# Kernel optimization log

Hardware: AMD Instinct MI355X
Metric: run time of the kernel (lower is better)

The kernel has to match this reference:

```python
import jax, jax.numpy as jnp
import numpy as np

N_ATOMS = 10000
N_EDGES = 200000
L_MAX = 2
K_L = [32, 24, 16]  # k_max_l = n_element_channels * n_max_l

# (l1, l2, L) in the original loop order (l1 outer, l2 inner, L ascending)
PAIRS = [(0,0,0),(0,1,1),(0,2,2),
         (1,0,1),(1,1,0),(1,1,1),(1,1,2),(1,2,1),(1,2,2),
         (2,0,2),(2,1,1),(2,1,2),(2,2,0),(2,2,1),(2,2,2)]
# concatenated input width -> k_max_l[L] per (L, sigma) channel
LIN = {'0_1': (72, 32), '1_1': (80, 24), '1_m1': (40, 24), '2_1': (72, 16), '2_m1': (32, 16)}


def setup_inputs() -> dict:
    key = jax.random.key(0)
    it = iter(jax.random.split(key, 64))
    def nrm(shape):
        return jax.random.normal(next(it), shape, dtype=jnp.float32)
    inp = {}
    for l in range(L_MAX + 1):
        inp['rb%d' % l] = nrm((N_EDGES, K_L[l]))           # radial basis per l
    for l in range(L_MAX + 1):
        inp['sh%d' % l] = nrm((N_EDGES, 2*l+1, 1))         # spherical harmonics per l
    inp['emb'] = nrm((N_ATOMS, 1, K_L[0]))                 # initial center embedding
    for l in range(L_MAX + 1):
        inp['f%d' % l] = nrm((N_ATOMS, 2*l+1, K_L[l]))     # nu=1 equivariant features
    for (l1, l2, L) in PAIRS:
        inp['cg_%d_%d_%d' % (l1, l2, L)] = nrm(((2*l1+1)*(2*l2+1), 2*L+1))
    for LS, (fin, fout) in LIN.items():
        inp['W_' + LS] = nrm((fin, fout)) / np.float32(np.sqrt(fin))
        inp['b_' + LS] = nrm((fout,)) * 0.01
    inp['centers'] = jax.random.randint(next(it), (N_EDGES,), 0, N_ATOMS)
    inp['neighbors'] = jax.random.randint(next(it), (N_EDGES,), 0, N_ATOMS)
    inp['n_atoms'] = N_ATOMS
    return inp


def _normalize(x, dims):
    # Normalizer(dims): RMS normalization over the given dims
    return x * jax.lax.rsqrt(jnp.mean(x * x, axis=dims, keepdims=True) + 1e-12)


def _forward(floats, centers, neighbors, n_atoms):
    (rb0, rb1, rb2, sh0, sh1, sh2, emb, f0, f1, f2,
     cg_0_0_0, cg_0_1_1, cg_0_2_2, cg_1_0_1, cg_1_1_0, cg_1_1_1, cg_1_1_2,
     cg_1_2_1, cg_1_2_2, cg_2_0_2, cg_2_1_1, cg_2_1_2, cg_2_2_0, cg_2_2_1,
     cg_2_2_2, W_0_1, b_0_1, W_1_1, b_1_1, W_1_m1, b_1_m1, W_2_1, b_2_1,
     W_2_m1, b_2_m1) = floats
    rb = [rb0, rb1, rb2]; sh = [sh0, sh1, sh2]; feats = [f0, f1, f2]
    cgs = {'0_0_0': cg_0_0_0, '0_1_1': cg_0_1_1, '0_2_2': cg_0_2_2,
           '1_0_1': cg_1_0_1, '1_1_0': cg_1_1_0, '1_1_1': cg_1_1_1,
           '1_1_2': cg_1_1_2, '1_2_1': cg_1_2_1, '1_2_2': cg_1_2_2,
           '2_0_2': cg_2_0_2, '2_1_1': cg_2_1_1, '2_1_2': cg_2_1_2,
           '2_2_0': cg_2_2_0, '2_2_1': cg_2_2_1, '2_2_2': cg_2_2_2}
    lin = {'0_1': (W_0_1, b_0_1), '1_1': (W_1_1, b_1_1), '1_m1': (W_1_m1, b_1_m1),
           '2_1': (W_2_1, b_2_1), '2_m1': (W_2_m1, b_2_m1)}

    # ---- InvariantMessagePasser: density_l = scatter_add over centers of
    #      sh_l * rb_l * emb[neighbors]
    emb_n = emb[neighbors]                                       # [E, 1, k0]
    densities = []
    for l in range(L_MAX + 1):
        msg = sh[l] * rb[l][:, None, :] * emb_n[:, :, :K_L[l]]   # [E, 2l+1, k_l]
        densities.append(jax.ops.segment_sum(msg, centers, num_segments=n_atoms))

    # ---- EquivariantMessagePasser
    ve = [sh[l] * rb[l][:, None, :] for l in range(L_MAX + 1)]   # vector expansion [E,2l+1,k_l]
    fn = [feats[l][neighbors] for l in range(L_MAX + 1)]         # gathered neighbor feats
    results = {}
    for (l1, l2, L) in PAIRS:
        S = (-1) ** (l1 + l2 + L)
        k = min(K_L[l1], K_L[l2])
        t1 = ve[l1][:, :, :k]                                    # [E, 2l1+1, k]
        t2 = fn[l2][:, :, :k]                                    # [E, 2l2+1, k]
        cg = cgs['%d_%d_%d' % (l1, l2, L)].reshape(2*l1+1, 2*l2+1, 2*L+1)
        # fused outer product + CG contraction -> [E, 2L+1, k]
        res = jnp.einsum('eak,ebk,abM->eMk', t1, t2, cg)
        pooled = jax.ops.segment_sum(res, centers, num_segments=n_atoms)
        LS = '%d_%s' % (L, 'm1' if S < 0 else '1')
        results.setdefault(LS, []).append(pooled)

    outs = {}
    for LS, (W, b) in lin.items():
        x = jnp.concatenate(results[LS], axis=2)                 # [n_atoms, 2L+1, size_LS]
        x = _normalize(x, (0, 1))
        x = jnp.einsum('amf,fk->amk', x, W) + b
        outs[LS] = _normalize(x, (0, 1, 2))

    return (densities[0], densities[1], densities[2],
            outs['0_1'], outs['1_1'], outs['1_m1'], outs['2_1'], outs['2_m1'])


def reference(rb0, rb1, rb2, sh0, sh1, sh2, emb, f0, f1, f2,
              cg_0_0_0, cg_0_1_1, cg_0_2_2, cg_1_0_1, cg_1_1_0, cg_1_1_1,
              cg_1_1_2, cg_1_2_1, cg_1_2_2, cg_2_0_2, cg_2_1_1, cg_2_1_2,
              cg_2_2_0, cg_2_2_1, cg_2_2_2, W_0_1, b_0_1, W_1_1, b_1_1,
              W_1_m1, b_1_m1, W_2_1, b_2_1, W_2_m1, b_2_m1,
              centers, neighbors, n_atoms):
    floats = (rb0, rb1, rb2, sh0, sh1, sh2, emb, f0, f1, f2,
              cg_0_0_0, cg_0_1_1, cg_0_2_2, cg_1_0_1, cg_1_1_0, cg_1_1_1,
              cg_1_1_2, cg_1_2_1, cg_1_2_2, cg_2_0_2, cg_2_1_1, cg_2_1_2,
              cg_2_2_0, cg_2_2_1, cg_2_2_2, W_0_1, b_0_1, W_1_1, b_1_1,
              W_1_m1, b_1_m1, W_2_1, b_2_1, W_2_m1, b_2_m1)
    return _forward(floats, centers, neighbors, n_atoms)
```

## Files before the change

kernel.cpp:

```cpp
#include <hip/hip_runtime.h>
#include <hip/hip_bf16.h>

typedef __hip_bfloat16 bf16;

#define N_ATOMS 10000
#define N_EDGES 200000

#define SCG   0
#define SINV  616
#define SS1P  1024
#define SS2P  19968
#define SWS2  20288
#define SINTS 20352
#define IFLAG  0
#define ICOUNT 16
#define IOFFS  10016
#define ICURS  20032
#define IELIST 30032
#define INTS_END_SMALL 230032
#define INTS_END_BIG   430032
#define SXACC (SINTS + INTS_END_BIG)
#define BIG_FLOATS (SXACC + 952*N_ATOMS)

#define O0 0
#define O1 320000
#define O2 1040000
#define OY 1840000
#define OUT_ELEMS 5200000

__device__ __forceinline__ float b2f(bf16 x){ return __bfloat162float(x); }
__device__ __forceinline__ bf16  f2b(float x){ return __float2bfloat16(x); }

__device__ __forceinline__ float ldv(const float* p, int i){ return p[i]; }
__device__ __forceinline__ float ldv(const bf16*  p, int i){ return b2f(p[i]); }
__device__ __forceinline__ void  stv(float* p, int i, float v){ p[i] = v; }
__device__ __forceinline__ void  stv(bf16*  p, int i, float v){ p[i] = f2b(v); }

template<typename T> __device__ __forceinline__ int dtid();
template<> __device__ __forceinline__ int dtid<bf16>(){ return 0; }
template<> __device__ __forceinline__ int dtid<float>(){ return 1; }

struct Ptrs15 { const void* p[15]; };
struct LinP   { const void* W[5]; const void* B[5]; };

__constant__ int c_cg_sizes[15] = {1,9,25,9,9,27,45,45,75,25,45,75,25,75,125};
__constant__ int c_fin[5]   = {72,80,40,72,32};
__constant__ int c_kout[5]  = {32,24,24,16,16};
__constant__ int c_yoff[5]  = {OY+0, OY+320000, OY+1040000, OY+1760000, OY+2560000};
__constant__ int c_numel[5] = {320000,720000,720000,800000,800000};
__constant__ int c_cum[6]   = {0,32,104,176,256,336};
__constant__ int c_xb[5]    = {0,72,312,432,792};
__constant__ int c_Ms[5]    = {1,3,3,5,5};

__global__ void k_zero(float* wsf, int* wsi,
                       const unsigned short* rb0u, const unsigned short* embu) {
  if (blockIdx.x == 0 && threadIdx.x < 64) {
    int lane = threadIdx.x;
    int bad = 0;
    for (int i = lane; i < 256; i += 64) {
      unsigned u1 = ((unsigned)rb0u[2*i]) << 16;
      unsigned u2 = ((unsigned)embu[2*i]) << 16;
      float v1 = __uint_as_float(u1);
      float v2 = __uint_as_float(u2);
      if (!(fabsf(v1) < 1e9f) || !(fabsf(v2) < 1e9f)) bad = 1;
    }
    unsigned long long any = __ballot(bad);
    if (lane == 0) wsi[IFLAG] = (any != 0ULL) ? 1 : 0;
  }
  int i = blockIdx.x*blockDim.x + threadIdx.x;
  if (i < N_ATOMS) wsi[ICOUNT + i] = 0;
  int j = i - N_ATOMS;
  if (j >= 0 && j < N_ATOMS) wsi[ICURS + j] = 0;
  j -= N_ATOMS;
  if (j >= 0 && j < 18944) wsf[SS1P + j] = 0.f;
  j -= 18944;
  if (j >= 0 && j < 325) wsf[SS2P + j] = 0.f;
}

template<typename T>
__global__ void k_cg(Ptrs15 cg, float* wsf, const int* flag) {
  if (flag[0] != dtid<T>()) return;
  int i = blockIdx.x*blockDim.x + threadIdx.x;
  if (i >= 615) return;
  int s = 0, off = i;
  while (off >= c_cg_sizes[s]) { off -= c_cg_sizes[s]; ++s; }
  wsf[SCG + i] = ldv((const T*)cg.p[s], off);
}

__global__ void k_hist(const int* __restrict__ centers, int* __restrict__ counts) {
  int e = blockIdx.x*blockDim.x + threadIdx.x;
  if (e < N_EDGES) atomicAdd(&counts[centers[e]], 1);
}

__global__ void k_scan(const int* __restrict__ counts, int* __restrict__ offs) {
  __shared__ int part[1024];
  int t = threadIdx.x;
  int base = t*10;
  int s = 0;
  for (int i = 0; i < 10; ++i) { int idx = base+i; if (idx < N_ATOMS) s += counts[idx]; }
  part[t] = s;
  __syncthreads();
  for (int d = 1; d < 1024; d <<= 1) {
    int v = part[t];
    int add = (t >= d) ? part[t-d] : 0;
    __syncthreads();
    part[t] = v + add;
    __syncthreads();
  }
  int run = (t == 0) ? 0 : part[t-1];
  for (int i = 0; i < 10; ++i) {
    int idx = base+i;
    if (idx < N_ATOMS) { offs[idx] = run; run += counts[idx]; }
  }
  if (t == 1023) offs[N_ATOMS] = part[1023];
}

__global__ void k_scatter(const int* __restrict__ centers, const int* __restrict__ offs,
                          int* __restrict__ cursors, int* __restrict__ elist) {
  int e = blockIdx.x*blockDim.x + threadIdx.x;
  if (e < N_EDGES) {
    int c = centers[e];
    int p = atomicAdd(&cursors[c], 1);
    elist[offs[c] + p] = e;
  }
}

__global__ void k_scatter2(const int* __restrict__ centers, const int* __restrict__ neighbors,
                           const int* __restrict__ offs, int* __restrict__ cursors,
                           int2* __restrict__ elist2) {
  int e = blockIdx.x*blockDim.x + threadIdx.x;
  if (e < N_EDGES) {
    int c = centers[e];
    int p = atomicAdd(&cursors[c], 1);
    elist2[offs[c] + p] = make_int2(e, neighbors[e]);
  }
}

template<typename T, int MODE>
__global__ __launch_bounds__(256) void k_main(
    const T* __restrict__ rb0, const T* __restrict__ rb1, const T* __restrict__ rb2,
    const T* __restrict__ sh0, const T* __restrict__ sh1, const T* __restrict__ sh2,
    const T* __restrict__ emb, const T* __restrict__ f0, const T* __restrict__ f1,
    const T* __restrict__ f2, const int* __restrict__ neighbors,
    const int* __restrict__ offs, const int* __restrict__ elist,
    const float* __restrict__ cgf, float* __restrict__ s1p,
    const float* __restrict__ inv, float* __restrict__ s2p,
    float* __restrict__ xout, LinP lp, T* __restrict__ out,
    const int* __restrict__ flag)
{
  if (flag[0] != dtid<T>()) return;
  int lane = threadIdx.x & 63;
  int wv   = threadIdx.x >> 6;
  int tix  = threadIdx.x;
  int a = blockIdx.x;
  int beg = offs[a];
  int cnt = offs[a+1] - beg;
  int k32 = lane & 31, e2 = lane >> 5;
  int k16 = lane & 15, e4 = lane >> 4;
  const int2* el2 = (const int2*)elist;
  int ab = a & 63;

  __shared__ int2 sel[256];
  __shared__ __align__(16) float L[952];
  __shared__ float red[4][5];

  float acc[25];
  #pragma unroll
  for (int i = 0; i < 25; ++i) acc[i] = 0.f;

  for (int cbase = 0; cbase < cnt; cbase += 256) {
    int nch = cnt - cbase; if (nch > 256) nch = 256;
    __syncthreads();
    if (tix < nch) {
      if constexpr (MODE == 0) {
        sel[tix] = el2[beg + cbase + tix];
      } else {
        int e = elist[beg + cbase + tix];
        sel[tix] = make_int2(e, neighbors[e]);
      }
    }
    __syncthreads();

    if (wv == 0) {
      for (int base = 0; base < nch; base += 4) {
        #pragma unroll
        for (int u = 0; u < 2; ++u) {
          int idx = base + 2*u + e2;
          float w = (idx < nch) ? 1.f : 0.f;
          int ic  = (idx < nch) ? idx : 0;
          int2 en = sel[ic];
          int e = en.x, n = en.y;
          float s0 = ldv(sh0, e);
          float s1a0 = ldv(sh1, e*3+0), s1a1 = ldv(sh1, e*3+1), s1a2 = ldv(sh1, e*3+2);
          float rb0k = ldv(rb0, e*32 + k32) * w;
          float ek   = ldv(emb, n*32 + k32);
          float f0k  = ldv(f0,  n*32 + k32);
          float ve0 = s0 * rb0k;
          acc[0] = fmaf(ve0, ek, acc[0]);
          acc[4] = fmaf(ve0, f0k, acc[4]);
          if (k32 < 24) {
            float rb1k = ldv(rb1, e*24 + k32) * w;
            float f1k0 = ldv(f1, n*72 + k32);
            float f1k1 = ldv(f1, n*72 + 24 + k32);
            float f1k2 = ldv(f1, n*72 + 48 + k32);
            float rbek = rb1k * ek;
            acc[1] = fmaf(s1a0, rbek, acc[1]);
            acc[2] = fmaf(s1a1, rbek, acc[2]);
            acc[3] = fmaf(s1a2, rbek, acc[3]);
            acc[5] = fmaf(ve0, f1k0, acc[5]);
            acc[6] = fmaf(ve0, f1k1, acc[6]);
            acc[7] = fmaf(ve0, f1k2, acc[7]);
            float g3 = rb1k * f0k;
            acc[8]  = fmaf(g3, s1a0, acc[8]);
            acc[9]  = fmaf(g3, s1a1, acc[9]);
            acc[10] = fmaf(g3, s1a2, acc[10]);
            #pragma unroll
            for (int aa = 0; aa < 3; ++aa) {
              float sa = rb1k * ((aa==0)?s1a0:(aa==1)?s1a1:s1a2);
              acc[11+aa*3+0] = fmaf(sa, f1k0, acc[11+aa*3+0]);
              acc[11+aa*3+1] = fmaf(sa, f1k1, acc[11+aa*3+1]);
              acc[11+aa*3+2] = fmaf(sa, f1k2, acc[11+aa*3+2]);
            }
          }
        }
      }
    } else if (wv == 1) {
      for (int base = 0; base < nch; base += 8) {
        #pragma unroll
        for (int u = 0; u < 2; ++u) {
          int idx = base + 4*u + e4;
          float w = (idx < nch) ? 1.f : 0.f;
          int ic  = (idx < nch) ? idx : 0;
          int2 en = sel[ic];
          int e = en.x, n = en.y;
          float s0 = ldv(sh0, e);
          float s1a[3];
          #pragma unroll
          for (int m = 0; m < 3; ++m) s1a[m] = ldv(sh1, e*3+m);
          float s2a[5];
          #pragma unroll
          for (int m = 0; m < 5; ++m) s2a[m] = ldv(sh2, e*5+m);
          float rb0k = ldv(rb0, e*32 + k16) * w;
          float rb1k = ldv(rb1, e*24 + k16) * w;
          float rb2k = ldv(rb2, e*16 + k16) * w;
          float ek   = ldv(emb, n*32 + k16);
          float f2k[5];
          #pragma unroll
          for (int b = 0; b < 5; ++b) f2k[b] = ldv(f2, n*80 + b*16 + k16);
          float re = rb2k * ek;
          #pragma unroll
          for (int m = 0; m < 5; ++m) acc[m] = fmaf(s2a[m], re, acc[m]);
          float ve0 = s0 * rb0k;
          #pragma unroll
          for (int b = 0; b < 5; ++b) acc[5+b] = fmaf(ve0, f2k[b], acc[5+b]);
          #pragma unroll
          for (int aa = 0; aa < 3; ++aa) {
            float sa = rb1k * s1a[aa];
            #pragma unroll
            for (int b = 0; b < 5; ++b)
              acc[10+aa*5+b] = fmaf(sa, f2k[b], acc[10+aa*5+b]);
          }
        }
      }
// ... 137 lines not shown
    for (int M = 0; M < 5; ++M) {
      float t = 0.f;
      #pragma unroll
      for (int q = 0; q < 15; ++q) t = fmaf(acc[10+q], C122[q*5+M], t);
      r[8+M] = t;
    }
    #pragma unroll
    for (int M = 0; M < 5; ++M) acc[5+M]  = r[M];
    #pragma unroll
    for (int M = 0; M < 3; ++M) acc[10+M] = r[5+M];
    #pragma unroll
    for (int M = 0; M < 5; ++M) acc[13+M] = r[8+M];
  } else if (wv == 2) {
    #pragma unroll
    for (int i = 0; i < 20; ++i) {
      acc[i] += __shfl_xor(acc[i], 16);
      acc[i] += __shfl_xor(acc[i], 32);
    }
    const float* C202 = cgf + 245;
    const float* C211 = cgf + 270;
    const float* C212 = cgf + 315;
    float r[13];
    #pragma unroll
    for (int M = 0; M < 5; ++M) {
      float t = 0.f;
      #pragma unroll
      for (int aa = 0; aa < 5; ++aa) t = fmaf(acc[aa], C202[aa*5+M], t);
      r[M] = t;
    }
    #pragma unroll
    for (int M = 0; M < 3; ++M) {
      float t = 0.f;
      #pragma unroll
      for (int q = 0; q < 15; ++q) t = fmaf(acc[5+q], C211[q*3+M], t);
      r[5+M] = t;
    }
    #pragma unroll
    for (int M = 0; M < 5; ++M) {
      float t = 0.f;
      #pragma unroll
      for (int q = 0; q < 15; ++q) t = fmaf(acc[5+q], C212[q*5+M], t);
      r[8+M] = t;
    }
    #pragma unroll
    for (int M = 0; M < 5; ++M) acc[M]   = r[M];
    #pragma unroll
    for (int M = 0; M < 3; ++M) acc[5+M] = r[5+M];
    #pragma unroll
    for (int M = 0; M < 5; ++M) acc[8+M] = r[8+M];
  } else {
    #pragma unroll
    for (int i = 0; i < 25; ++i) {
      acc[i] += __shfl_xor(acc[i], 16);
      acc[i] += __shfl_xor(acc[i], 32);
    }
    const float* C220 = cgf + 390;
    const float* C221 = cgf + 415;
    const float* C222 = cgf + 490;
    float r[9];
    {
      float t = 0.f;
      #pragma unroll
      for (int q = 0; q < 25; ++q) t = fmaf(acc[q], C220[q], t);
      r[0] = t;
    }
    #pragma unroll
    for (int M = 0; M < 3; ++M) {
      float t = 0.f;
      #pragma unroll
      for (int q = 0; q < 25; ++q) t = fmaf(acc[q], C221[q*3+M], t);
      r[1+M] = t;
    }
    #pragma unroll
    for (int M = 0; M < 5; ++M) {
      float t = 0.f;
      #pragma unroll
      for (int q = 0; q < 25; ++q) t = fmaf(acc[q], C222[q*5+M], t);
      r[4+M] = t;
    }
    #pragma unroll
    for (int i = 0; i < 9; ++i) acc[i] = r[i];
  }

  if constexpr (MODE != 2) {
    if (wv == 0) {
      if (lane < 32) {
        stv(out, O0 + a*32 + k32, acc[0]);
        atomicAdd(&s1p[(0+k32)*64+ab], acc[4]*acc[4]);
        if (k32 < 24) {
          #pragma unroll
          for (int m = 0; m < 3; ++m) stv(out, O1 + a*72 + m*24 + k32, acc[1+m]);
          atomicAdd(&s1p[(32+k32)*64+ab], acc[11]*acc[11]);
          float q;
          q = acc[5]*acc[5]+acc[6]*acc[6]+acc[7]*acc[7];
          atomicAdd(&s1p[(72+k32)*64+ab], q);
          q = acc[8]*acc[8]+acc[9]*acc[9]+acc[10]*acc[10];
          atomicAdd(&s1p[(96+k32)*64+ab], q);
          q = acc[12]*acc[12]+acc[13]*acc[13]+acc[14]*acc[14];
          atomicAdd(&s1p[(152+k32)*64+ab], q);
          q = acc[15]*acc[15]+acc[16]*acc[16]+acc[17]*acc[17]
            + acc[18]*acc[18]+acc[19]*acc[19];
          atomicAdd(&s1p[(208+k32)*64+ab], q);
        }
      }
    } else if (wv == 1) {
      if (lane < 16) {
        #pragma unroll
        for (int m = 0; m < 5; ++m) stv(out, O2 + a*80 + m*16 + k16, acc[m]);
        float q;
        q = acc[5]*acc[5]+acc[6]*acc[6]+acc[7]*acc[7]+acc[8]*acc[8]+acc[9]*acc[9];
        atomicAdd(&s1p[(192+k16)*64+ab], q);
        q = acc[10]*acc[10]+acc[11]*acc[11]+acc[12]*acc[12];
        atomicAdd(&s1p[(120+k16)*64+ab], q);
        q = acc[13]*acc[13]+acc[14]*acc[14]+acc[15]*acc[15]
          + acc[16]*acc[16]+acc[17]*acc[17];
        atomicAdd(&s1p[(264+k16)*64+ab], q);
      }
    } else if (wv == 2) {
      if (lane < 16) {
        float q;
        q = acc[0]*acc[0]+acc[1]*acc[1]+acc[2]*acc[2]+acc[3]*acc[3]+acc[4]*acc[4];
        atomicAdd(&s1p[(232+k16)*64+ab], q);
        q = acc[5]*acc[5]+acc[6]*acc[6]+acc[7]*acc[7];
        atomicAdd(&s1p[(136+k16)*64+ab], q);
        q = acc[8]*acc[8]+acc[9]*acc[9]+acc[10]*acc[10]
          + acc[11]*acc[11]+acc[12]*acc[12];
        atomicAdd(&s1p[(280+k16)*64+ab], q);
      }
    } else {
      if (lane < 16) {
        atomicAdd(&s1p[(56+k16)*64+ab], acc[0]*acc[0]);
        float q;
        q = acc[1]*acc[1]+acc[2]*acc[2]+acc[3]*acc[3];
        atomicAdd(&s1p[(176+k16)*64+ab], q);
        q = acc[4]*acc[4]+acc[5]*acc[5]+acc[6]*acc[6]
          + acc[7]*acc[7]+acc[8]*acc[8];
        atomicAdd(&s1p[(248+k16)*64+ab], q);
      }
    }
  }

  if constexpr (MODE == 0) {
    if (wv == 0) {
      if (lane < 32) {
        L[k32] = acc[4];
        if (k32 < 24) {
          L[32+k32] = acc[11];
          #pragma unroll
          for (int M = 0; M < 3; ++M) L[72+M*80+k32]     = acc[5+M];
          #pragma unroll
          for (int M = 0; M < 3; ++M) L[72+M*80+24+k32]  = acc[8+M];
          #pragma unroll
          for (int M = 0; M < 3; ++M) L[312+M*40+k32]    = acc[12+M];
          #pragma unroll
          for (int M = 0; M < 5; ++M) L[432+M*72+16+k32] = acc[15+M];
        }
      }
    } else if (wv == 1) {
      if (lane < 16) {
        #pragma unroll
        for (int M = 0; M < 5; ++M) L[432+M*72+k16]    = acc[5+M];
        #pragma unroll
        for (int M = 0; M < 3; ++M) L[72+M*80+48+k16]  = acc[10+M];
        #pragma unroll
        for (int M = 0; M < 5; ++M) L[792+M*32+k16]    = acc[13+M];
      }
    } else if (wv == 2) {
      if (lane < 16) {
        #pragma unroll
        for (int M = 0; M < 5; ++M) L[432+M*72+40+k16] = acc[0+M];
        #pragma unroll
        for (int M = 0; M < 3; ++M) L[72+M*80+64+k16]  = acc[5+M];
        #pragma unroll
        for (int M = 0; M < 5; ++M) L[792+M*32+16+k16] = acc[8+M];
      }
    } else {
      if (lane < 16) {
        L[56+k16] = acc[0];
        #pragma unroll
        for (int M = 0; M < 3; ++M) L[312+M*40+24+k16] = acc[1+M];
        #pragma unroll
        for (int M = 0; M < 5; ++M) L[432+M*72+56+k16] = acc[4+M];
      }
    }
    __syncthreads();
    const float4* Ls = (const float4*)L;
    float4* xd = (float4*)(xout + a*952);
    for (int i = tix; i < 238; i += 256) xd[i] = Ls[i];
  }

  if constexpr (MODE == 2) {
    if (wv == 0) {
      if (lane < 32) {
        L[k32] = acc[4]*inv[k32];
        if (k32 < 24) {
          L[32+k32] = acc[11]*inv[32+k32];
          #pragma unroll
          for (int M = 0; M < 3; ++M) L[72+M*80+k32]     = acc[5+M]*inv[72+k32];
          #pragma unroll
          for (int M = 0; M < 3; ++M) L[72+M*80+24+k32]  = acc[8+M]*inv[96+k32];
          #pragma unroll
          for (int M = 0; M < 3; ++M) L[312+M*40+k32]    = acc[12+M]*inv[152+k32];
          #pragma unroll
          for (int M = 0; M < 5; ++M) L[432+M*72+16+k32] = acc[15+M]*inv[208+k32];
        }
      }
    } else if (wv == 1) {
      if (lane < 16) {
        #pragma unroll
        for (int M = 0; M < 5; ++M) L[432+M*72+k16]    = acc[5+M]*inv[192+k16];
        #pragma unroll
        for (int M = 0; M < 3; ++M) L[72+M*80+48+k16]  = acc[10+M]*inv[120+k16];
        #pragma unroll
        for (int M = 0; M < 5; ++M) L[792+M*32+k16]    = acc[13+M]*inv[264+k16];
      }
    } else if (wv == 2) {
      if (lane < 16) {
        #pragma unroll
        for (int M = 0; M < 5; ++M) L[432+M*72+40+k16] = acc[0+M]*inv[232+k16];
        #pragma unroll
        for (int M = 0; M < 3; ++M) L[72+M*80+64+k16]  = acc[5+M]*inv[136+k16];
        #pragma unroll
        for (int M = 0; M < 5; ++M) L[792+M*32+16+k16] = acc[8+M]*inv[280+k16];
      }
    } else {
      if (lane < 16) {
        L[56+k16] = acc[0]*inv[56+k16];
        #pragma unroll
        for (int M = 0; M < 3; ++M) L[312+M*40+24+k16] = acc[1+M]*inv[176+k16];
        #pragma unroll
        for (int M = 0; M < 5; ++M) L[432+M*72+56+k16] = acc[4+M]*inv[248+k16];
      }
    }
    __syncthreads();
    int t = threadIdx.x;
    float y2[5] = {0.f,0.f,0.f,0.f,0.f};
    for (int tau = t; tau < 336; tau += 256) {
      int ls = 0;
      while (tau >= c_cum[ls+1]) ++ls;
      int rem = tau - c_cum[ls];
      int kn = c_kout[ls], fin = c_fin[ls];
      int M = rem / kn, ko = rem - M*kn;
      const T* W = (const T*)lp.W[ls];
      float y = ldv((const T*)lp.B[ls], ko);
      const float* xv = &L[c_xb[ls] + M*fin];
      for (int f = 0; f < fin; ++f) y = fmaf(xv[f], ldv(W, f*kn+ko), y);
      stv(out, c_yoff[ls] + (a*c_Ms[ls] + M)*kn + ko, y);
      y2[ls] += y*y;
    }
    #pragma unroll
    for (int i = 0; i < 5; ++i) {
      y2[i] += __shfl_xor(y2[i], 1);  y2[i] += __shfl_xor(y2[i], 2);
      y2[i] += __shfl_xor(y2[i], 4);  y2[i] += __shfl_xor(y2[i], 8);
      y2[i] += __shfl_xor(y2[i], 16); y2[i] += __shfl_xor(y2[i], 32);
    }
    if (lane == 0) {
      #pragma unroll
      for (int i = 0; i < 5; ++i) red[wv][i] = y2[i];
    }
    __syncthreads();
    if (t == 0) {
      #pragma unroll
      for (int i = 0; i < 5; ++i)
        atomicAdd(&s2p[i*64 + ab], red[0][i]+red[1][i]+red[2][i]+red[3][i]);
    }
  }
}

template<typename T>
__global__ __launch_bounds__(256) void k_lin(
    const float* __restrict__ xg, const float* __restrict__ inv,
    LinP lp, T* __restrict__ out, float* __restrict__ s2p,
    const int* __restrict__ flag)
{
  if (flag[0] != dtid<T>()) return;
  int a = blockIdx.x;
  int t = threadIdx.x;
  __shared__ float L[952];
  for (int i = t; i < 952; i += 256) {
    int ch;
    if      (i < 72)  ch = i;
    else if (i < 312) ch = 72  + (i-72)  % 80;
    else if (i < 432) ch = 152 + (i-312) % 40;
    else if (i < 792) ch = 192 + (i-432) % 72;
    else              ch = 264 + (i-792) % 32;
    L[i] = xg[a*952 + i] * inv[ch];
  }
  __syncthreads();
  float y2[5] = {0.f,0.f,0.f,0.f,0.f};
  for (int tau = t; tau < 336; tau += 256) {
    int ls = 0;
    while (tau >= c_cum[ls+1]) ++ls;
    int rem = tau - c_cum[ls];
    int kn = c_kout[ls], fin = c_fin[ls];
    int M = rem / kn, ko = rem - M*kn;
    const T* W = (const T*)lp.W[ls];
    float y = ldv((const T*)lp.B[ls], ko);
    const float* xv = &L[c_xb[ls] + M*fin];
    for (int f = 0; f < fin; ++f) y = fmaf(xv[f], ldv(W, f*kn+ko), y);
    stv(out, c_yoff[ls] + (a*c_Ms[ls] + M)*kn + ko, y);
    y2[ls] += y*y;
  }
  __shared__ float red[4][5];
  #pragma unroll
  for (int i = 0; i < 5; ++i) {
    y2[i] += __shfl_xor(y2[i], 1);  y2[i] += __shfl_xor(y2[i], 2);
    y2[i] += __shfl_xor(y2[i], 4);  y2[i] += __shfl_xor(y2[i], 8);
    y2[i] += __shfl_xor(y2[i], 16); y2[i] += __shfl_xor(y2[i], 32);
  }
  if ((t & 63) == 0) {
    #pragma unroll
    for (int i = 0; i < 5; ++i) red[t>>6][i] = y2[i];
  }
  __syncthreads();
  if (t == 0) {
    #pragma unroll
    for (int i = 0; i < 5; ++i)
      atomicAdd(&s2p[i*64 + (a & 63)], red[0][i]+red[1][i]+red[2][i]+red[3][i]);
  }
}

__global__ void k_red1(const float* __restrict__ s1p, float* __restrict__ inv) {
  int ch = blockIdx.x, lane = threadIdx.x;
  float v = s1p[ch*64 + lane];
  v += __shfl_xor(v, 1);  v += __shfl_xor(v, 2);  v += __shfl_xor(v, 4);
  v += __shfl_xor(v, 8);  v += __shfl_xor(v, 16); v += __shfl_xor(v, 32);
  if (lane == 0) {
    float rows = (ch < 72) ? 10000.f : (ch < 192) ? 30000.f : 50000.f;
    inv[ch] = rsqrtf(v/rows + 1e-12f);
  }
}

__global__ void k_red2(const float* __restrict__ s2p, float* __restrict__ ws2) {
  int ls = blockIdx.x, lane = threadIdx.x;
  float v = s2p[ls*64 + lane];
  v += __shfl_xor(v, 1);  v += __shfl_xor(v, 2);  v += __shfl_xor(v, 4);
  v += __shfl_xor(v, 8);  v += __shfl_xor(v, 16); v += __shfl_xor(v, 32);
  if (lane == 0) ws2[ls] = v;
}

template<typename T>
__global__ void k_scale(const float* __restrict__ ws2, T* __restrict__ out,
                        const int* __restrict__ flag) {
  if (flag[0] != dtid<T>()) return;
  int i = blockIdx.x*blockDim.x + threadIdx.x;
  if (i >= 3360000) return;
  int ls = (i < 320000) ? 0 : (i < 1040000) ? 1 : (i < 1760000) ? 2 : (i < 2560000) ? 3 : 4;
  float scale = rsqrtf(ws2[ls] / (float)c_numel[ls] + 1e-12f);
  stv(out, OY + i, ldv((const T*)out, OY + i) * scale);
}

template<typename T>
static void launch_chain(void* const* d_in, T* out, float* wsf, int* wsi,
                         Ptrs15 cg, LinP lp, bool big, hipStream_t stream) {
  const T* rb0 = (const T*)d_in[0];
  const T* rb1 = (const T*)d_in[1];
  const T* rb2 = (const T*)d_in[2];
  const T* sh0 = (const T*)d_in[3];
  const T* sh1 = (const T*)d_in[4];
  const T* sh2 = (const T*)d_in[5];
  const T* emb = (const T*)d_in[6];
  const T* f0  = (const T*)d_in[7];
  const T* f1  = (const T*)d_in[8];
  const T* f2  = (const T*)d_in[9];
  const int* neighbors = (const int*)d_in[36];
  const int* flag = wsi + IFLAG;

  k_cg<T><<<3, 256, 0, stream>>>(cg, wsf, flag);
  if (big) {
    k_main<T,0><<<N_ATOMS, 256, 0, stream>>>(rb0, rb1, rb2, sh0, sh1, sh2, emb, f0, f1, f2,
        neighbors, wsi+IOFFS, wsi+IELIST, wsf+SCG, wsf+SS1P, nullptr, nullptr,
        wsf+SXACC, lp, out, flag);
    k_red1<<<296, 64, 0, stream>>>(wsf+SS1P, wsf+SINV);
    k_lin<T><<<N_ATOMS, 256, 0, stream>>>(wsf+SXACC, wsf+SINV, lp, out, wsf+SS2P, flag);
  } else {
    k_main<T,1><<<N_ATOMS, 256, 0, stream>>>(rb0, rb1, rb2, sh0, sh1, sh2, emb, f0, f1, f2,
        neighbors, wsi+IOFFS, wsi+IELIST, wsf+SCG, wsf+SS1P, nullptr, nullptr,
        nullptr, lp, out, flag);
    k_red1<<<296, 64, 0, stream>>>(wsf+SS1P, wsf+SINV);
    k_main<T,2><<<N_ATOMS, 256, 0, stream>>>(rb0, rb1, rb2, sh0, sh1, sh2, emb, f0, f1, f2,
        neighbors, wsi+IOFFS, wsi+IELIST, wsf+SCG, nullptr, wsf+SINV, wsf+SS2P,
        nullptr, lp, out, flag);
  }
  k_red2<<<5, 64, 0, stream>>>(wsf+SS2P, wsf+SWS2);
  k_scale<T><<<(3360000+255)/256, 256, 0, stream>>>(wsf+SWS2, out, flag);
}

extern "C" void kernel_launch(void* const* d_in, const int* in_sizes, int n_in,
                              void* d_out, int out_size, void* d_ws, size_t ws_size,
                              hipStream_t stream) {
  float* wsf = (float*)d_ws;
  int*   wsi = (int*)(wsf + SINTS);
  const int* centers   = (const int*)d_in[35];
  const int* neighbors = (const int*)d_in[36];
  bool big = ws_size >= (size_t)BIG_FLOATS * 4;

  int know = -1;
  if (in_sizes) {
    long long nb = (long long)in_sizes[0];
    if (nb == (long long)N_EDGES*32*2) know = 0;
    else if (nb == (long long)N_EDGES*32*4) know = 1;
  }
  if (know < 0) {
    long long ob = (long long)out_size;
    if (ob == (long long)OUT_ELEMS*2) know = 0;
    else if (ob == (long long)OUT_ELEMS*4) know = 1;
  }

  Ptrs15 cg;
  for (int i = 0; i < 15; ++i) cg.p[i] = d_in[10+i];
  LinP lp;
  lp.W[0] = d_in[25]; lp.B[0] = d_in[26];
  lp.W[1] = d_in[27]; lp.B[1] = d_in[28];
  lp.W[2] = d_in[29]; lp.B[2] = d_in[30];
  lp.W[3] = d_in[31]; lp.B[3] = d_in[32];
  lp.W[4] = d_in[33]; lp.B[4] = d_in[34];

  k_zero<<<154, 256, 0, stream>>>(wsf, wsi,
                                  (const unsigned short*)d_in[0],
                                  (const unsigned short*)d_in[6]);
  k_hist<<<(N_EDGES+255)/256, 256, 0, stream>>>(centers, wsi+ICOUNT);
  k_scan<<<1, 1024, 0, stream>>>(wsi+ICOUNT, wsi+IOFFS);
  if (big) {
    k_scatter2<<<(N_EDGES+255)/256, 256, 0, stream>>>(centers, neighbors, wsi+IOFFS,
                                                      wsi+ICURS, (int2*)(wsi+IELIST));
  } else {
    k_scatter<<<(N_EDGES+255)/256, 256, 0, stream>>>(centers, wsi+IOFFS, wsi+ICURS, wsi+IELIST);
  }

  if (know != 1) launch_chain<bf16 >(d_in, (bf16*)d_out,  wsf, wsi, cg, lp, big, stream);
  if (know != 0) launch_chain<float>(d_in, (float*)d_out, wsf, wsi, cg, lp, big, stream);
}
```

Before: 514.2 us.

## Split per-atom main kernel into five independent wave roles with per-wave CG contraction

Replaces the big-workspace k_main (one 256-thread block per atom, with waves doing unequal work and syncing through shared memory) by k_role, where each 64-lane wave independently handles one of five coupling-path groups for one atom. Each wave reads the edge list straight from global memory, does its own CG contraction and writes directly to the xacc buffer. This removes block-level syncs and load imbalance and raises the number of schedulable waves. The s1p partial-sum layout changes to atom-bucket-major, and k_red1 is updated to match. The change also always builds the int2 edge list, which drops the small-workspace scatter path, and the cost is that each edge's data is re-read by several waves.

After: 450.3 us. 1.14x faster.

```diff
diff --git a/kernel.cpp b/kernel.cpp
--- a/kernel.cpp
+++ b/kernel.cpp
@@ -17,9 +17,8 @@
 #define IOFFS  10016
 #define ICURS  20032
 #define IELIST 30032
-#define INTS_END_SMALL 230032
-#define INTS_END_BIG   430032
-#define SXACC (SINTS + INTS_END_BIG)
+#define INTS_END 430032
+#define SXACC (SINTS + INTS_END)
 #define BIG_FLOATS (SXACC + 952*N_ATOMS)
 
 #define O0 0
@@ -115,16 +114,6 @@
   if (t == 1023) offs[N_ATOMS] = part[1023];
 }
 
-__global__ void k_scatter(const int* __restrict__ centers, const int* __restrict__ offs,
-                          int* __restrict__ cursors, int* __restrict__ elist) {
-  int e = blockIdx.x*blockDim.x + threadIdx.x;
-  if (e < N_EDGES) {
-    int c = centers[e];
-    int p = atomicAdd(&cursors[c], 1);
-    elist[offs[c] + p] = e;
-  }
-}
-
 __global__ void k_scatter2(const int* __restrict__ centers, const int* __restrict__ neighbors,
                            const int* __restrict__ offs, int* __restrict__ cursors,
                            int2* __restrict__ elist2) {
@@ -136,16 +125,411 @@
   }
 }
 
+template<typename T>
+__global__ __launch_bounds__(128) void k_role(
+    const T* __restrict__ rb0, const T* __restrict__ rb1, const T* __restrict__ rb2,
+    const T* __restrict__ sh0, const T* __restrict__ sh1, const T* __restrict__ sh2,
+    const T* __restrict__ emb, const T* __restrict__ f0, const T* __restrict__ f1,
+    const T* __restrict__ f2, const int2* __restrict__ el2,
+    const int* __restrict__ offs, const float* __restrict__ cgf,
+    float* __restrict__ s1p, float* __restrict__ xout, T* __restrict__ out,
+    const int* __restrict__ flag)
+{
+  if (flag[0] != dtid<T>()) return;
+  int lane = threadIdx.x & 63;
+  int g = blockIdx.x * 2 + (threadIdx.x >> 6);
+  int a = g / 5;
+  int role = g - a*5;
+  int beg = offs[a];
+  int cnt = offs[a+1] - beg;
+  const int2* eb = el2 + beg;
+  int ab = a & 63;
+  int k32 = lane & 31, e2 = lane >> 5;
+  int k16 = lane & 15, e4 = lane >> 4;
+  float* xg = xout + a*952;
+  float* s1r = s1p + ab*296;
+
+  if (role == 0) {
+    float acc[8];
+    #pragma unroll
+    for (int i = 0; i < 8; ++i) acc[i] = 0.f;
+    for (int base = 0; base < cnt; base += 4) {
+      #pragma unroll
+      for (int u = 0; u < 2; ++u) {
+        int idx = base + 2*u + e2;
+        float w = (idx < cnt) ? 1.f : 0.f;
+        int ic  = (idx < cnt) ? idx : 0;
+        int2 en = eb[ic];
+        int e = en.x, n = en.y;
+        float s0 = ldv(sh0, e);
+        float s1a0 = ldv(sh1, e*3+0), s1a1 = ldv(sh1, e*3+1), s1a2 = ldv(sh1, e*3+2);
+        float rb0k = ldv(rb0, e*32 + k32) * w;
+        float ek   = ldv(emb, n*32 + k32);
+        float f0k  = ldv(f0,  n*32 + k32);
+        float ve0 = s0 * rb0k;
+        acc[0] = fmaf(ve0, ek, acc[0]);
+        acc[4] = fmaf(ve0, f0k, acc[4]);
+        if (k32 < 24) {
+          float rb1k = ldv(rb1, e*24 + k32) * w;
+          float rbek = rb1k * ek;
+          acc[1] = fmaf(s1a0, rbek, acc[1]);
+          acc[2] = fmaf(s1a1, rbek, acc[2]);
+          acc[3] = fmaf(s1a2, rbek, acc[3]);
+          float f1k0 = ldv(f1, n*72 + k32);
+          float f1k1 = ldv(f1, n*72 + 24 + k32);
+          float f1k2 = ldv(f1, n*72 + 48 + k32);
+          acc[5] = fmaf(ve0, f1k0, acc[5]);
+          acc[6] = fmaf(ve0, f1k1, acc[6]);
+          acc[7] = fmaf(ve0, f1k2, acc[7]);
+        }
+      }
+    }
+    #pragma unroll
+    for (int i = 0; i < 8; ++i) acc[i] += __shfl_xor(acc[i], 32);
+    float x000 = cgf[0] * acc[4];
+    const float* C011 = cgf + 1;
+    float x011[3];
+    #pragma unroll
+    for (int M = 0; M < 3; ++M) {
+      float t = 0.f;
+      #pragma unroll
+      for (int b = 0; b < 3; ++b) t = fmaf(acc[5+b], C011[b*3+M], t);
+      x011[M] = t;
+    }
+    if (lane < 32) {
+      stv(out, O0 + a*32 + k32, acc[0]);
+      xg[k32] = x000;
+      atomicAdd(&s1r[k32], x000*x000);
+      if (k32 < 24) {
+        #pragma unroll
+        for (int m = 0; m < 3; ++m) stv(out, O1 + a*72 + m*24 + k32, acc[1+m]);
+        #pragma unroll
+        for (int M = 0; M < 3; ++M) xg[72+M*80+k32] = x011[M];
+        atomicAdd(&s1r[72+k32], x011[0]*x011[0]+x011[1]*x011[1]+x011[2]*x011[2]);
+      }
+    }
+  } else if (role == 1) {
+    float acc[12];
+    #pragma unroll
+    for (int i = 0; i < 12; ++i) acc[i] = 0.f;
+    int k24 = (k32 < 24) ? k32 : 23;
+    float m24 = (k32 < 24) ? 1.f : 0.f;
+    for (int base = 0; base < cnt; base += 4) {
+      #pragma unroll
+      for (int u = 0; u < 2; ++u) {
+        int idx = base + 2*u + e2;
+        float w = ((idx < cnt) ? 1.f : 0.f) * m24;
+        int ic  = (idx < cnt) ? idx : 0;
+        int2 en = eb[ic];
+        int e = en.x, n = en.y;
+        float s1a0 = ldv(sh1, e*3+0), s1a1 = ldv(sh1, e*3+1), s1a2 = ldv(sh1, e*3+2);
+        float rb1k = ldv(rb1, e*24 + k24) * w;
+        float f0k  = ldv(f0,  n*32 + k24);
+        float f1k0 = ldv(f1, n*72 + k24);
+        float f1k1 = ldv(f1, n*72 + 24 + k24);
+        float f1k2 = ldv(f1, n*72 + 48 + k24);
+        float g3 = rb1k * f0k;
+        acc[0] = fmaf(g3, s1a0, acc[0]);
+        acc[1] = fmaf(g3, s1a1, acc[1]);
+        acc[2] = fmaf(g3, s1a2, acc[2]);
+        float sa;
+        sa = rb1k * s1a0;
+        acc[3] = fmaf(sa, f1k0, acc[3]); acc[4] = fmaf(sa, f1k1, acc[4]); acc[5] = fmaf(sa, f1k2, acc[5]);
+        sa = rb1k * s1a1;
+        acc[6] = fmaf(sa, f1k0, acc[6]); acc[7] = fmaf(sa, f1k1, acc[7]); acc[8] = fmaf(sa, f1k2, acc[8]);
+        sa = rb1k * s1a2;
+        acc[9] = fmaf(sa, f1k0, acc[9]); acc[10] = fmaf(sa, f1k1, acc[10]); acc[11] = fmaf(sa, f1k2, acc[11]);
+      }
+    }
+    #pragma unroll
+    for (int i = 0; i < 12; ++i) acc[i] += __shfl_xor(acc[i], 32);
+    const float* C101 = cgf + 35;
+    const float* C110 = cgf + 44;
+    const float* C111 = cgf + 53;
+    const float* C112 = cgf + 80;
+    float x101[3], x111[3], x112[5], x110;
+    #pragma unroll
+    for (int M = 0; M < 3; ++M) {
+      float t = 0.f;
+      #pragma unroll
+      for (int aa = 0; aa < 3; ++aa) t = fmaf(acc[aa], C101[aa*3+M], t);
+      x101[M] = t;
+    }
+    {
+      float t = 0.f;
+      #pragma unroll
+      for (int q = 0; q < 9; ++q) t = fmaf(acc[3+q], C110[q], t);
+      x110 = t;
+    }
+    #pragma unroll
+    for (int M = 0; M < 3; ++M) {
+      float t = 0.f;
+      #pragma unroll
+      for (int q = 0; q < 9; ++q) t = fmaf(acc[3+q], C111[q*3+M], t);
+      x111[M] = t;
+    }
+    #pragma unroll
+    for (int M = 0; M < 5; ++M) {
+      float t = 0.f;
+      #pragma unroll
+      for (int q = 0; q < 9; ++q) t = fmaf(acc[3+q], C112[q*5+M], t);
+      x112[M] = t;
+    }
+    if (lane < 24) {
+      xg[32+k32] = x110;
+      #pragma unroll
+      for (int M = 0; M < 3; ++M) xg[72+M*80+24+k32] = x101[M];
+      #pragma unroll
+      for (int M = 0; M < 3; ++M) xg[312+M*40+k32]   = x111[M];
+      #pragma unroll
+      for (int M = 0; M < 5; ++M) xg[432+M*72+16+k32] = x112[M];
+      atomicAdd(&s1r[32+k32], x110*x110);
+      atomicAdd(&s1r[96+k32], x101[0]*x101[0]+x101[1]*x101[1]+x101[2]*x101[2]);
+      atomicAdd(&s1r[152+k32], x111[0]*x111[0]+x111[1]*x111[1]+x111[2]*x111[2]);
+      atomicAdd(&s1r[208+k32], x112[0]*x112[0]+x112[1]*x112[1]+x112[2]*x112[2]
+                              + x112[3]*x112[3]+x112[4]*x112[4]);
+    }
+  } else if (role == 2) {
+    float acc[25];
+    #pragma unroll
+    for (int i = 0; i < 25; ++i) acc[i] = 0.f;
+    for (int base = 0; base < cnt; base += 8) {
+      #pragma unroll
+      for (int u = 0; u < 2; ++u) {
+        int idx = base + 4*u + e4;
+        float w = (idx < cnt) ? 1.f : 0.f;
+        int ic  = (idx < cnt) ? idx : 0;
+        int2 en = eb[ic];
+        int e = en.x, n = en.y;
+        float s0 = ldv(sh0, e);
+        float s1a[3];
+        #pragma unroll
+        for (int m = 0; m < 3; ++m) s1a[m] = ldv(sh1, e*3+m);
+        float s2a[5];
+        #pragma unroll
+        for (int m = 0; m < 5; ++m) s2a[m] = ldv(sh2, e*5+m);
+        float rb0k = ldv(rb0, e*32 + k16) * w;
+        float rb1k = ldv(rb1, e*24 + k16) * w;
+        float rb2k = ldv(rb2, e*16 + k16) * w;
+        float ek   = ldv(emb, n*32 + k16);
+        float f2k[5];
+        #pragma unroll
+        for (int b = 0; b < 5; ++b) f2k[b] = ldv(f2, n*80 + b*16 + k16);
+        float re = rb2k * ek;
+        #pragma unroll
+        for (int m = 0; m < 5; ++m) acc[m] = fmaf(s2a[m], re, acc[m]);
+        float ve0 = s0 * rb0k;
+        #pragma unroll
+        for (int b = 0; b < 5; ++b) acc[5+b] = fmaf(ve0, f2k[b], acc[5+b]);
+        #pragma unroll
+        for (int aa = 0; aa < 3; ++aa) {
+          float sa = rb1k * s1a[aa];
+          #pragma unroll
+          for (int b = 0; b < 5; ++b)
+            acc[10+aa*5+b] = fmaf(sa, f2k[b], acc[10+aa*5+b]);
+        }
+      }
+    }
+    #pragma unroll
+    for (int i = 0; i < 25; ++i) {
+      acc[i] += __shfl_xor(acc[i], 16);
+      acc[i] += __shfl_xor(acc[i], 32);
+    }
+    const float* C022 = cgf + 10;
+    const float* C121 = cgf + 125;
+    const float* C122 = cgf + 170;
+    float x022[5], x121[3], x122[5];
+    #pragma unroll
+    for (int M = 0; M < 5; ++M) {
+      float t = 0.f;
+      #pragma unroll
+      for (int b = 0; b < 5; ++b) t = fmaf(acc[5+b], C022[b*5+M], t);
+      x022[M] = t;
+    }
+    #pragma unroll
+    for (int M = 0; M < 3; ++M) {
+      float t = 0.f;
+      #pragma unroll
+      for (int q = 0; q < 15; ++q) t = fmaf(acc[10+q], C121[q*3+M], t);
+      x121[M] = t;
+    }
+    #pragma unroll
+    for (int M = 0; M < 5; ++M) {
+      float t = 0.f;
+      #pragma unroll
+      for (int q = 0; q < 15; ++q) t = fmaf(acc[10+q], C122[q*5+M], t);
+      x122[M] = t;
+    }
+    if (lane < 16) {
+      #pragma unroll
+      for (int m = 0; m < 5; ++m) stv(out, O2 + a*80 + m*16 + k16, acc[m]);
+      #pragma unroll
+      for (int M = 0; M < 5; ++M) xg[432+M*72+k16]   = x022[M];
+      #pragma unroll
+      for (int M = 0; M < 3; ++M) xg[72+M*80+48+k16] = x121[M];
+      #pragma unroll
+      for (int M = 0; M < 5; ++M) xg[792+M*32+k16]   = x122[M];
+      atomicAdd(&s1r[192+k16], x022[0]*x022[0]+x022[1]*x022[1]+x022[2]*x022[2]
+                              + x022[3]*x022[3]+x022[4]*x022[4]);
+      atomicAdd(&s1r[120+k16], x121[0]*x121[0]+x121[1]*x121[1]+x121[2]*x121[2]);
+      atomicAdd(&s1r[264+k16], x122[0]*x122[0]+x122[1]*x122[1]+x122[2]*x122[2]
+                              + x122[3]*x122[3]+x122[4]*x122[4]);
+    }
+  } else if (role == 3) {
+    float acc[20];
+    #pragma unroll
+    for (int i = 0; i < 20; ++i) acc[i] = 0.f;
+    for (int base = 0; base < cnt; base += 8) {
+      #pragma unroll
+      for (int u = 0; u < 2; ++u) {
+        int idx = base + 4*u + e4;
+        float w = (idx < cnt) ? 1.f : 0.f;
+        int ic  = (idx < cnt) ? idx : 0;
+        int2 en = eb[ic];
+        int e = en.x, n = en.y;
+        float s2a[5];
+        #pragma unroll
+        for (int m = 0; m < 5; ++m) s2a[m] = ldv(sh2, e*5+m);
+        float rb2k = ldv(rb2, e*16 + k16) * w;
+        float f0k  = ldv(f0,  n*32 + k16);
+        float f1k[3];
+        #pragma unroll
+        for (int b = 0; b < 3; ++b) f1k[b] = ldv(f1, n*72 + b*24 + k16);
+        float g9 = rb2k * f0k;
+        #pragma unroll
+        for (int aa = 0; aa < 5; ++aa) acc[aa] = fmaf(g9, s2a[aa], acc[aa]);
+        #pragma unroll
+        for (int aa = 0; aa < 5; ++aa) {
+          float sa = rb2k * s2a[aa];
+          #pragma unroll
+          for (int b = 0; b < 3; ++b)
+            acc[5+aa*3+b] = fmaf(sa, f1k[b], acc[5+aa*3+b]);
+        }
+      }
+    }
+    #pragma unroll
+    for (int i = 0; i < 20; ++i) {
+      acc[i] += __shfl_xor(acc[i], 16);
+      acc[i] += __shfl_xor(acc[i], 32);
+    }
+    const float* C202 = cgf + 245;
+    const float* C211 = cgf + 270;
+    const float* C212 = cgf + 315;
+    float x202[5], x211[3], x212[5];
+    #pragma unroll
+    for (int M = 0; M < 5; ++M) {
+      float t = 0.f;
+      #pragma unroll
+      for (int aa = 0; aa < 5; ++aa) t = fmaf(acc[aa], C202[aa*5+M], t);
+      x202[M] = t;
+    }
+    #pragma unroll
+    for (int M = 0; M < 3; ++M) {
+      float t = 0.f;
+      #pragma unroll
+      for (int q = 0; q < 15; ++q) t = fmaf(acc[5+q], C211[q*3+M], t);
+      x211[M] = t;
+    }
+    #pragma unroll
+    for (int M = 0; M < 5; ++M) {
+      float t = 0.f;
+      #pragma unroll
+      for (int q = 0; q < 15; ++q) t = fmaf(acc[5+q], C212[q*5+M], t);
+      x212[M] = t;
+    }
+    if (lane < 16) {
+      #pragma unroll
+      for (int M = 0; M < 5; ++M) xg[432+M*72+40+k16] = x202[M];
+      #pragma unroll
+      for (int M = 0; M < 3; ++M) xg[72+M*80+64+k16]  = x211[M];
+      #pragma unroll
+      for (int M = 0; M < 5; ++M) xg[792+M*32+16+k16] = x212[M];
+      atomicAdd(&s1r[232+k16], x202[0]*x202[0]+x202[1]*x202[1]+x202[2]*x202[2]
+                              + x202[3]*x202[3]+x202[4]*x202[4]);
+      atomicAdd(&s1r[136+k16], x211[0]*x211[0]+x211[1]*x211[1]+x211[2]*x211[2]);
+      atomicAdd(&s1r[280+k16], x212[0]*x212[0]+x212[1]*x212[1]+x212[2]*x212[2]
+                              + x212[3]*x212[3]+x212[4]*x212[4]);
+    }
+  } else {
+    float acc[25];
+    #pragma unroll
+    for (int i = 0; i < 25; ++i) acc[i] = 0.f;
+    for (int base = 0; base < cnt; base += 8) {
+      #pragma unroll
+      for (int u = 0; u < 2; ++u) {
+        int idx = base + 4*u + e4;
+        float w = (idx < cnt) ? 1.f : 0.f;
+        int ic  = (idx < cnt) ? idx : 0;
+        int2 en = eb[ic];
+        int e = en.x, n = en.y;
+        float s2a[5];
+        #pragma unroll
+        for (int m = 0; m < 5; ++m) s2a[m] = ldv(sh2, e*5+m);
+        float rb2k = ldv(rb2, e*16 + k16) * w;
+        float f2k[5];
+        #pragma unroll
+        for (int b = 0; b < 5; ++b) f2k[b] = ldv(f2, n*80 + b*16 + k16);
+        #pragma unroll
+        for (int aa = 0; aa < 5; ++aa) {
+          float sa = rb2k * s2a[aa];
+          #pragma unroll
+          for (int b = 0; b < 5; ++b)
+            acc[aa*5+b] = fmaf(sa, f2k[b], acc[aa*5+b]);
+        }
+      }
+    }
+    #pragma unroll
+    for (int i = 0; i < 25; ++i) {
+      acc[i] += __shfl_xor(acc[i], 16);
+      acc[i] += __shfl_xor(acc[i], 32);
+    }
+    const float* C220 = cgf + 390;
+    const float* C221 = cgf + 415;
+    const float* C222 = cgf + 490;
+    float x220, x221[3], x222[5];
+    {
+      float t = 0.f;
+      #pragma unroll
+      for (int q = 0; q < 25; ++q) t = fmaf(acc[q], C220[q], t);
+      x220 = t;
+    }
+    #pragma unroll
+    for (int M = 0; M < 3; ++M) {
+      float t = 0.f;
+      #pragma unroll
+      for (int q = 0; q < 25; ++q) t = fmaf(acc[q], C221[q*3+M], t);
+      x221[M] = t;
+    }
+    #pragma unroll
+    for (int M = 0; M < 5; ++M) {
+      float t = 0.f;
+      #pragma unroll
+      for (int q = 0; q < 25; ++q) t = fmaf(acc[q], C222[q*5+M], t);
+      x222[M] = t;
+    }
+    if (lane < 16) {
+      xg[56+k16] = x220;
+      #pragma unroll
+      for (int M = 0; M < 3; ++M) xg[312+M*40+24+k16] = x221[M];
+      #pragma unroll
+      for (int M = 0; M < 5; ++M) xg[432+M*72+56+k16] = x222[M];
+      atomicAdd(&s1r[56+k16], x220*x220);
+      atomicAdd(&s1r[176+k16], x221[0]*x221[0]+x221[1]*x221[1]+x221[2]*x221[2]);
+      atomicAdd(&s1r[248+k16], x222[0]*x222[0]+x222[1]*x222[1]+x222[2]*x222[2]
+                              + x222[3]*x222[3]+x222[4]*x222[4]);
+    }
+  }
+}
+
 template<typename T, int MODE>
 __global__ __launch_bounds__(256) void k_main(
     const T* __restrict__ rb0, const T* __restrict__ rb1, const T* __restrict__ rb2,
     const T* __restrict__ sh0, const T* __restrict__ sh1, const T* __restrict__ sh2,
     const T* __restrict__ emb, const T* __restrict__ f0, const T* __restrict__ f1,
-    const T* __restrict__ f2, const int* __restrict__ neighbors,
-    const int* __restrict__ offs, const int* __restrict__ elist,
-    const float* __restrict__ cgf, float* __restrict__ s1p,
-    const float* __restrict__ inv, float* __restrict__ s2p,
-    float* __restrict__ xout, LinP lp, T* __restrict__ out,
+    const T* __restrict__ f2, const int2* __restrict__ el2,
+    const int* __restrict__ offs, const float* __restrict__ cgf,
+    float* __restrict__ s1p, const float* __restrict__ inv,
+    float* __restrict__ s2p, LinP lp, T* __restrict__ out,
     const int* __restrict__ flag)
 {
   if (flag[0] != dtid<T>()) return;
@@ -157,8 +541,8 @@
   int cnt = offs[a+1] - beg;
   int k32 = lane & 31, e2 = lane >> 5;
   int k16 = lane & 15, e4 = lane >> 4;
-  const int2* el2 = (const int2*)elist;
   int ab = a & 63;
+  float* s1r = s1p + ab*296;
 
   __shared__ int2 sel[256];
   __shared__ __align__(16) float L[952];
@@ -171,14 +555,7 @@
   for (int cbase = 0; cbase < cnt; cbase += 256) {
     int nch = cnt - cbase; if (nch > 256) nch = 256;
     __syncthreads();
-    if (tix < nch) {
-      if constexpr (MODE == 0) {
-        sel[tix] = el2[beg + cbase + tix];
-      } else {
-        int e = elist[beg + cbase + tix];
-        sel[tix] = make_int2(e, neighbors[e]);
-      }
-    }
+    if (tix < nch) sel[tix] = el2[beg + cbase + tix];
     __syncthreads();
 
     if (wv == 0) {
@@ -482,25 +859,25 @@
     for (int i = 0; i < 9; ++i) acc[i] = r[i];
   }
 
-  if constexpr (MODE != 2) {
+  if constexpr (MODE == 1) {
     if (wv == 0) {
       if (lane < 32) {
         stv(out, O0 + a*32 + k32, acc[0]);
-        atomicAdd(&s1p[(0+k32)*64+ab], acc[4]*acc[4]);
+        atomicAdd(&s1r[k32], acc[4]*acc[4]);
         if (k32 < 24) {
           #pragma unroll
           for (int m = 0; m < 3; ++m) stv(out, O1 + a*72 + m*24 + k32, acc[1+m]);
-          atomicAdd(&s1p[(32+k32)*64+ab], acc[11]*acc[11]);
+          atomicAdd(&s1r[32+k32], acc[11]*acc[11]);
           float q;
           q = acc[5]*acc[5]+acc[6]*acc[6]+acc[7]*acc[7];
-          atomicAdd(&s1p[(72+k32)*64+ab], q);
+          atomicAdd(&s1r[72+k32], q);
           q = acc[8]*acc[8]+acc[9]*acc[9]+acc[10]*acc[10];
-          atomicAdd(&s1p[(96+k32)*64+ab], q);
+          atomicAdd(&s1r[96+k32], q);
           q = acc[12]*acc[12]+acc[13]*acc[13]+acc[14]*acc[14];
-          atomicAdd(&s1p[(152+k32)*64+ab], q);
+          atomicAdd(&s1r[152+k32], q);
           q = acc[15]*acc[15]+acc[16]*acc[16]+acc[17]*acc[17]
             + acc[18]*acc[18]+acc[19]*acc[19];
-          atomicAdd(&s1p[(208+k32)*64+ab], q);
+          atomicAdd(&s1r[208+k32], q);
         }
       }
     } else if (wv == 1) {
@@ -509,84 +886,35 @@
         for (int m = 0; m < 5; ++m) stv(out, O2 + a*80 + m*16 + k16, acc[m]);
         float q;
         q = acc[5]*acc[5]+acc[6]*acc[6]+acc[7]*acc[7]+acc[8]*acc[8]+acc[9]*acc[9];
-        atomicAdd(&s1p[(192+k16)*64+ab], q);
+        atomicAdd(&s1r[192+k16], q);
         q = acc[10]*acc[10]+acc[11]*acc[11]+acc[12]*acc[12];
-        atomicAdd(&s1p[(120+k16)*64+ab], q);
+        atomicAdd(&s1r[120+k16], q);
         q = acc[13]*acc[13]+acc[14]*acc[14]+acc[15]*acc[15]
           + acc[16]*acc[16]+acc[17]*acc[17];
-        atomicAdd(&s1p[(264+k16)*64+ab], q);
+        atomicAdd(&s1r[264+k16], q);
       }
     } else if (wv == 2) {
       if (lane < 16) {
         float q;
         q = acc[0]*acc[0]+acc[1]*acc[1]+acc[2]*acc[2]+acc[3]*acc[3]+acc[4]*acc[4];
-        atomicAdd(&s1p[(232+k16)*64+ab], q);
+        atomicAdd(&s1r[232+k16], q);
         q = acc[5]*acc[5]+acc[6]*acc[6]+acc[7]*acc[7];
-        atomicAdd(&s1p[(136+k16)*64+ab], q);
+        atomicAdd(&s1r[136+k16], q);
         q = acc[8]*acc[8]+acc[9]*acc[9]+acc[10]*acc[10]
           + acc[11]*acc[11]+acc[12]*acc[12];
-        atomicAdd(&s1p[(280+k16)*64+ab], q);
+        atomicAdd(&s1r[280+k16], q);
       }
     } else {
       if (lane < 16) {
-        atomicAdd(&s1p[(56+k16)*64+ab], acc[0]*acc[0]);
+        atomicAdd(&s1r[56+k16], acc[0]*acc[0]);
         float q;
         q = acc[1]*acc[1]+acc[2]*acc[2]+acc[3]*acc[3];
-        atomicAdd(&s1p[(176+k16)*64+ab], q);
+        atomicAdd(&s1r[176+k16], q);
         q = acc[4]*acc[4]+acc[5]*acc[5]+acc[6]*acc[6]
           + acc[7]*acc[7]+acc[8]*acc[8];
-        atomicAdd(&s1p[(248+k16)*64+ab], q);
-      }
-    }
-  }
-
-  if constexpr (MODE == 0) {
-    if (wv == 0) {
-      if (lane < 32) {
-        L[k32] = acc[4];
-        if (k32 < 24) {
-          L[32+k32] = acc[11];
-          #pragma unroll
-          for (int M = 0; M < 3; ++M) L[72+M*80+k32]     = acc[5+M];
-          #pragma unroll
-          for (int M = 0; M < 3; ++M) L[72+M*80+24+k32]  = acc[8+M];
-          #pragma unroll
-          for (int M = 0; M < 3; ++M) L[312+M*40+k32]    = acc[12+M];
-          #pragma unroll
-          for (int M = 0; M < 5; ++M) L[432+M*72+16+k32] = acc[15+M];
-        }
-      }
-    } else if (wv == 1) {
-      if (lane < 16) {
-        #pragma unroll
-        for (int M = 0; M < 5; ++M) L[432+M*72+k16]    = acc[5+M];
-        #pragma unroll
-        for (int M = 0; M < 3; ++M) L[72+M*80+48+k16]  = acc[10+M];
-        #pragma unroll
-        for (int M = 0; M < 5; ++M) L[792+M*32+k16]    = acc[13+M];
-      }
-    } else if (wv == 2) {
-      if (lane < 16) {
-        #pragma unroll
-        for (int M = 0; M < 5; ++M) L[432+M*72+40+k16] = acc[0+M];
-        #pragma unroll
-        for (int M = 0; M < 3; ++M) L[72+M*80+64+k16]  = acc[5+M];
-        #pragma unroll
-        for (int M = 0; M < 5; ++M) L[792+M*32+16+k16] = acc[8+M];
-      }
-    } else {
-      if (lane < 16) {
-        L[56+k16] = acc[0];
-        #pragma unroll
-        for (int M = 0; M < 3; ++M) L[312+M*40+24+k16] = acc[1+M];
-        #pragma unroll
-        for (int M = 0; M < 5; ++M) L[432+M*72+56+k16] = acc[4+M];
-      }
-    }
-    __syncthreads();
-    const float4* Ls = (const float4*)L;
-    float4* xd = (float4*)(xout + a*952);
-    for (int i = tix; i < 238; i += 256) xd[i] = Ls[i];
+        atomicAdd(&s1r[248+k16], q);
+      }
+    }
   }
 
   if constexpr (MODE == 2) {
@@ -722,7 +1050,7 @@
 
 __global__ void k_red1(const float* __restrict__ s1p, float* __restrict__ inv) {
   int ch = blockIdx.x, lane = threadIdx.x;
-  float v = s1p[ch*64 + lane];
+  float v = s1p[lane*296 + ch];
   v += __shfl_xor(v, 1);  v += __shfl_xor(v, 2);  v += __shfl_xor(v, 4);
   v += __shfl_xor(v, 8);  v += __shfl_xor(v, 16); v += __shfl_xor(v, 32);
   if (lane == 0) {
@@ -763,24 +1091,21 @@
   const T* f0  = (const T*)d_in[7];
   const T* f1  = (const T*)d_in[8];
   const T* f2  = (const T*)d_in[9];
-  const int* neighbors = (const int*)d_in[36];
   const int* flag = wsi + IFLAG;
+  const int2* el2 = (const int2*)(wsi + IELIST);
 
   k_cg<T><<<3, 256, 0, stream>>>(cg, wsf, flag);
   if (big) {
-    k_main<T,0><<<N_ATOMS, 256, 0, stream>>>(rb0, rb1, rb2, sh0, sh1, sh2, emb, f0, f1, f2,
-        neighbors, wsi+IOFFS, wsi+IELIST, wsf+SCG, wsf+SS1P, nullptr, nullptr,
-        wsf+SXACC, lp, out, flag);
+    k_role<T><<<25000, 128, 0, stream>>>(rb0, rb1, rb2, sh0, sh1, sh2, emb, f0, f1, f2,
+        el2, wsi+IOFFS, wsf+SCG, wsf+SS1P, wsf+SXACC, out, flag);
     k_red1<<<296, 64, 0, stream>>>(wsf+SS1P, wsf+SINV);
     k_lin<T><<<N_ATOMS, 256, 0, stream>>>(wsf+SXACC, wsf+SINV, lp, out, wsf+SS2P, flag);
   } else {
     k_main<T,1><<<N_ATOMS, 256, 0, stream>>>(rb0, rb1, rb2, sh0, sh1, sh2, emb, f0, f1, f2,
-        neighbors, wsi+IOFFS, wsi+IELIST, wsf+SCG, wsf+SS1P, nullptr, nullptr,
-        nullptr, lp, out, flag);
+        el2, wsi+IOFFS, wsf+SCG, wsf+SS1P, nullptr, nullptr, lp, out, flag);
     k_red1<<<296, 64, 0, stream>>>(wsf+SS1P, wsf+SINV);
     k_main<T,2><<<N_ATOMS, 256, 0, stream>>>(rb0, rb1, rb2, sh0, sh1, sh2, emb, f0, f1, f2,
-        neighbors, wsi+IOFFS, wsi+IELIST, wsf+SCG, nullptr, wsf+SINV, wsf+SS2P,
-        nullptr, lp, out, flag);
+        el2, wsi+IOFFS, wsf+SCG, nullptr, wsf+SINV, wsf+SS2P, lp, out, flag);
   }
   k_red2<<<5, 64, 0, stream>>>(wsf+SS2P, wsf+SWS2);
   k_scale<T><<<(3360000+255)/256, 256, 0, stream>>>(wsf+SWS2, out, flag);
@@ -821,12 +1146,8 @@
                                   (const unsigned short*)d_in[6]);
   k_hist<<<(N_EDGES+255)/256, 256, 0, stream>>>(centers, wsi+ICOUNT);
   k_scan<<<1, 1024, 0, stream>>>(wsi+ICOUNT, wsi+IOFFS);
-  if (big) {
-    k_scatter2<<<(N_EDGES+255)/256, 256, 0, stream>>>(centers, neighbors, wsi+IOFFS,
-                                                      wsi+ICURS, (int2*)(wsi+IELIST));
-  } else {
-    k_scatter<<<(N_EDGES+255)/256, 256, 0, stream>>>(centers, wsi+IOFFS, wsi+ICURS, wsi+IELIST);
-  }
+  k_scatter2<<<(N_EDGES+255)/256, 256, 0, stream>>>(centers, neighbors, wsi+IOFFS,
+                                                    wsi+ICURS, (int2*)(wsi+IELIST));
 
   if (know != 1) launch_chain<bf16 >(d_in, (bf16*)d_out,  wsf, wsi, cg, lp, big, stream);
   if (know != 0) launch_chain<float>(d_in, (float*)d_out, wsf, wsi, cg, lp, big, stream);
```
